# Kernel optimization log

Measured on AMD Instinct MI355X. Metric: run time of the kernel, lower is better.

## Reference

```python
import jax, jax.numpy as jnp
import numpy as np

HEADS = 8
DIM_HEAD = 64
SCALE = DIM_HEAD ** -0.5


def setup_inputs() -> dict:
    key = jax.random.key(0)
    k1, k2, k3 = jax.random.split(key, 3)
    B, N, D = 4, 2048, HEADS * DIM_HEAD  # D = inner_dim = 512
    x = jax.random.normal(k1, (B, N, D), dtype=jnp.float32)
    # nn.Linear weights stored transposed vs torch; here we use [in, out]
    w_qkv = jax.random.normal(k2, (D, 3 * D), dtype=jnp.float32) * (D ** -0.5)
    w_out = jax.random.normal(k3, (D, D), dtype=jnp.float32) * (D ** -0.5)
    b_out = jnp.zeros((D,), dtype=jnp.float32)
    return {"x": x, "w_qkv": w_qkv, "w_out": w_out, "b_out": b_out}


def reference(x, w_qkv, w_out, b_out):
    B, N, D = x.shape
    qkv = x @ w_qkv  # [B, N, 3D]
    q, k, v = jnp.split(qkv, 3, axis=-1)

    def to_heads(t):  # b n (h d) -> b h n d
        return t.reshape(B, N, HEADS, DIM_HEAD).transpose(0, 2, 1, 3)

    q, k, v = to_heads(q), to_heads(k), to_heads(v)
    dots = jnp.einsum('bhnd,bhmd->bhnm', q, k) * SCALE  # [B,H,N,N]
    attn = jax.nn.softmax(dots, axis=-1)
    out = jnp.einsum('bhnm,bhmd->bhnd', attn, v)  # [B,H,N,d]
    out = out.transpose(0, 2, 1, 3).reshape(B, N, D)  # b h n d -> b n (h d)
    return out @ w_out + b_out
```

## Files before the change

### kernel.cpp

```cpp
#include <hip/hip_runtime.h>

typedef __bf16 bf16;
typedef __bf16 bf16x8 __attribute__((ext_vector_type(8)));
typedef __bf16 bf16x4 __attribute__((ext_vector_type(4)));
typedef float f32x4 __attribute__((ext_vector_type(4)));
typedef float f32x16 __attribute__((ext_vector_type(16)));
typedef unsigned int uint2v __attribute__((ext_vector_type(2)));

#define MFMA16(a, b, c) __builtin_amdgcn_mfma_f32_16x16x32_bf16(a, b, c, 0, 0, 0)
#define MFMA32(a, b, c) __builtin_amdgcn_mfma_f32_32x32x16_bf16(a, b, c, 0, 0, 0)

#define CS 0.18033688011112042f

#if __has_builtin(__builtin_amdgcn_exp2f)
#define EXP2(x) __builtin_amdgcn_exp2f(x)
#else
#define EXP2(x) exp2f(x)
#endif

#define WAIT_VM0() __builtin_amdgcn_s_waitcnt(0x0F70)
#define WAIT_VM3() __builtin_amdgcn_s_waitcnt(0x0F73)
#define WAIT_VM4() __builtin_amdgcn_s_waitcnt(0x0F74)
#define WAIT_VM6() __builtin_amdgcn_s_waitcnt(0x0F76)
#define WAIT_VM8() __builtin_amdgcn_s_waitcnt(0x0F78)

#define BARRIER() __builtin_amdgcn_s_barrier()
#define CFENCE() asm volatile("" ::: "memory")

__device__ __forceinline__ void load_lds16(const bf16* g, bf16* l) {
    __builtin_amdgcn_global_load_lds(
        (const __attribute__((address_space(1))) unsigned int*)g,
        (__attribute__((address_space(3))) unsigned int*)l, 16, 0, 0);
}

#if __has_builtin(__builtin_amdgcn_permlane32_swap)
__device__ __forceinline__ bf16x8 build_bfrag(bf16x4 plo, bf16x4 phi, int ) {
    union { bf16x4 b; unsigned int i[2]; } ul, uh;
    ul.b = plo; uh.b = phi;
    uint2v r0 = __builtin_amdgcn_permlane32_swap(ul.i[0], uh.i[0], false, false);
    uint2v r1 = __builtin_amdgcn_permlane32_swap(ul.i[1], uh.i[1], false, false);
    union { unsigned int i[4]; bf16x8 b; } ub;
    ub.i[0] = r0[0]; ub.i[1] = r1[0]; ub.i[2] = r0[1]; ub.i[3] = r1[1];
    return ub.b;
}

__device__ __forceinline__ float sum_halves(float x) {
    union { float f; unsigned int u; } a; a.f = x;
    uint2v r = __builtin_amdgcn_permlane32_swap(a.u, a.u, false, false);
    union { unsigned int u; float f; } b0, b1;
    b0.u = r[0]; b1.u = r[1];
    return b0.f + b1.f;
}
#else
__device__ __forceinline__ bf16x4 shfl_xor32_b64(bf16x4 v) {
    union { bf16x4 b; int i[2]; } u;
    u.b = v;
    u.i[0] = __shfl_xor(u.i[0], 32, 64);
    u.i[1] = __shfl_xor(u.i[1], 32, 64);
    return u.b;
}
__device__ __forceinline__ bf16x8 build_bfrag(bf16x4 plo, bf16x4 phi, int h) {
    bf16x4 xlo = shfl_xor32_b64(plo);
    bf16x4 xhi = shfl_xor32_b64(phi);
    bf16x4 lo4 = h ? xhi : plo;
    bf16x4 hi4 = h ? phi : xlo;
    bf16x8 bb;
#pragma unroll
    for (int i = 0; i < 4; ++i) { bb[i] = lo4[i]; bb[4 + i] = hi4[i]; }
    return bb;
}
__device__ __forceinline__ float sum_halves(float x) {
    return x + __shfl_xor(x, 32, 64);
}
#endif

__global__ __launch_bounds__(256) void prep_kernel(const float* __restrict__ x,
                                                   const float* __restrict__ w_qkv,
                                                   const float* __restrict__ w_out,
                                                   bf16* __restrict__ xb,
                                                   bf16* __restrict__ wqkvT,
                                                   bf16* __restrict__ woutT) {
    __shared__ float tile[32][33];
    int bid = blockIdx.x, t = threadIdx.x;
    if (bid < 4096) {
        int i = (bid * 256 + t) * 4;
        float4 v = *(const float4*)&x[i];
        bf16x4 o = {(bf16)v.x, (bf16)v.y, (bf16)v.z, (bf16)v.w};
        *(bf16x4*)&xb[i] = o;
        return;
    }
    const float* in; bf16* out; int C, bx, by;
    if (bid < 4864) { int b2 = bid - 4096; in = w_qkv; out = wqkvT; C = 1536; bx = b2 % 48; by = b2 / 48; }
    else            { int b3 = bid - 4864; in = w_out; out = woutT; C = 512;  bx = b3 & 15; by = b3 >> 4; }
    const int R = 512;
    int tx = t & 31, ty = t >> 5;
    int c0 = bx * 32, r0 = by * 32;
#pragma unroll
    for (int i = ty; i < 32; i += 8)
        tile[i][tx] = in[(size_t)(r0 + i) * C + c0 + tx];
    __syncthreads();
#pragma unroll
    for (int i = ty; i < 32; i += 8)
        out[(size_t)(c0 + i) * R + r0 + tx] = (bf16)tile[tx][i];
}

template <int MT, int BK, int NBUF, int MODE, typename OutT>
__global__ __launch_bounds__(256, 2)
void gemm_bt_kernel(const bf16* __restrict__ A,
                    const bf16* __restrict__ Bt,
                    const float* __restrict__ bias,
                    OutT* __restrict__ C,
                    bf16* __restrict__ vtout,
                    int M, int N, int K) {
    const int BM = MT * 32;
    const int CPR = BK / 8;
    const int ASZ = BM * BK, BSZ = 128 * BK;
    const int ALD = ASZ / 2048, BLD = BSZ / 2048;
    const int L = ALD + BLD;
    __shared__ bf16 As[NBUF * ASZ];
    __shared__ bf16 Bs[NBUF * BSZ];
    int t = threadIdx.x;
    int lane = t & 63, w = t >> 6;
    int wr = w >> 1, wc = w & 1;
    int quad = lane >> 4, r16 = lane & 15;

    int lin = blockIdx.y * gridDim.x + blockIdx.x;
    int cpx = (gridDim.x * gridDim.y) >> 3;
    int nl = (lin & 7) * cpx + (lin >> 3);
    int bx = nl % gridDim.x, by = nl / gridDim.x;
    int m0 = by * BM, n0 = bx * 128;

    const f32x4 fzero = {0.f, 0.f, 0.f, 0.f};
    f32x4 acc[MT][4];
#pragma unroll
    for (int i = 0; i < MT; ++i)
#pragma unroll
        for (int j = 0; j < 4; ++j) acc[i][j] = fzero;

    const bf16* ap[ALD]; bf16* ad[ALD];
    const bf16* bp[BLD]; bf16* bd[BLD];
#pragma unroll
    for (int i = 0; i < ALD; ++i) {
        int ci = i * 256 + t;
        int row = ci / CPR, cp = ci % CPR, cc = cp ^ (row & (CPR - 1));
        ap[i] = &A[(size_t)(m0 + row) * K + cc * 8];
        ad[i] = &As[ci * 8];
    }
#pragma unroll
    for (int i = 0; i < BLD; ++i) {
        int ci = i * 256 + t;
        int row = ci / CPR, cp = ci % CPR, cc = cp ^ (row & (CPR - 1));
        bp[i] = &Bt[(size_t)(n0 + row) * K + cc * 8];
        bd[i] = &Bs[ci * 8];
    }

    auto stage = [&](int par) {
#pragma unroll
        for (int i = 0; i < ALD; ++i) { load_lds16(ap[i], ad[i] + par * ASZ); ap[i] += BK; }
#pragma unroll
        for (int i = 0; i < BLD; ++i) { load_lds16(bp[i], bd[i] + par * BSZ); bp[i] += BK; }
    };

    int nk = K / BK;
#pragma unroll
    for (int p = 0; p < NBUF - 1; ++p) stage(p);
    int cur = 0, nxt = NBUF - 1;
    for (int kk = 0; kk < nk; ++kk) {
        int rem = nk - 1 - kk;
        if (rem >= NBUF - 1) {
            stage(nxt);
            nxt = (nxt + 1 == NBUF) ? 0 : nxt + 1;
            if constexpr (L * (NBUF - 1) == 3) WAIT_VM3();
            else if constexpr (L * (NBUF - 1) == 4) WAIT_VM4();
            else if constexpr (L * (NBUF - 1) == 6) WAIT_VM6();
            else WAIT_VM8();
        } else if (NBUF == 3 && rem == 1) {
            if constexpr (L == 3) WAIT_VM3(); else WAIT_VM4();
        } else {
            WAIT_VM0();
        }
        CFENCE(); BARRIER(); CFENCE();

        const bf16* Asb = &As[cur * ASZ];
        const bf16* Bsb = &Bs[cur * BSZ];
#pragma unroll
        for (int ks = 0; ks < BK / 32; ++ks) {
            bf16x8 af[MT], bfr[4];
            int swz = (ks * 4 + quad) ^ (r16 & (CPR - 1));
#pragma unroll
            for (int mt = 0; mt < MT; ++mt)
                af[mt] = *(const bf16x8*)&Asb[(wr * (BM / 2) + mt * 16 + r16) * BK + swz * 8];
#pragma unroll
            for (int nt = 0; nt < 4; ++nt)
                bfr[nt] = *(const bf16x8*)&Bsb[(wc * 64 + nt * 16 + r16) * BK + swz * 8];
#pragma unroll
            for (int mt = 0; mt < MT; ++mt)
#pragma unroll
                for (int nt = 0; nt < 4; ++nt)
                    acc[mt][nt] = MFMA16(af[mt], bfr[nt], acc[mt][nt]);
        }
        cur = (cur + 1 == NBUF) ? 0 : cur + 1;
        if (kk + 1 < nk) { CFENCE(); BARRIER(); CFENCE(); }
    }
#pragma unroll
    for (int mt = 0; mt < MT; ++mt)
#pragma unroll
        for (int nt = 0; nt < 4; ++nt) {
            int col = n0 + wc * 64 + nt * 16 + r16;
            int row0 = m0 + wr * (BM / 2) + mt * 16 + quad * 4;
            if (MODE == 1 && n0 >= 1024) {
                int dg = col - 1024, hh = dg >> 6, d = dg & 63;
                int bb = row0 >> 11, n = row0 & 2047;
                bf16x4 o;
#pragma unroll
                for (int r = 0; r < 4; ++r) o[r] = (bf16)acc[mt][nt][r];
                *(bf16x4*)&vtout[((size_t)((bb << 3) | hh) * 64 + d) * 2048 + n] = o;
            } else {
#pragma unroll
                for (int r = 0; r < 4; ++r) {
                    float v = acc[mt][nt][r];
                    if (MODE == 1 && n0 < 512) v *= CS;
                    if (MODE == 2) v += bias[col];
                    C[(size_t)(row0 + r) * N + col] = (OutT)v;
                }
            }
        }
}

__global__ __launch_bounds__(128, 2) void attn_kernel(const bf16* __restrict__ qkv,
                                                      const bf16* __restrict__ vt,
                                                      bf16* __restrict__ out) {
    __shared__ __align__(16) char smemraw[32768];
    bf16* stage = (bf16*)smemraw;

    int t = threadIdx.x;
    int lane = t & 63, w = t >> 6;
    int h = lane >> 5, q = lane & 31;
    int bh = blockIdx.y, b = bh >> 3, hd = bh & 7;
    int qb = blockIdx.x * 64;

    bf16x8 qf[2][4];
#pragma unroll
    for (int sub = 0; sub < 2; ++sub) {
        size_t qoff = (size_t)(b * 2048 + qb + sub * 32 + q) * 1536 + hd * 64;
#pragma unroll
        for (int s = 0; s < 4; ++s)
            qf[sub][s] = *(const bf16x8*)&qkv[qoff + s * 16 + h * 8];
    }

    f32x16 o_acc[2][2];
#pragma unroll
    for (int sub = 0; sub < 2; ++sub)
#pragma unroll
        for (int db = 0; db < 2; ++db)
#pragma unroll
            for (int i = 0; i < 16; ++i) o_acc[sub][db][i] = 0.f;
    float psum[2] = {0.f, 0.f};

    bf16* base = stage + w * 8192;

    const bf16* kp[4]; const bf16* vp[4];
    int kdo[4], vdo[4];
#pragma unroll
    for (int rdd = 0; rdd < 4; ++rdd) {
        int ciK = rdd * 64 + lane;
        int rowK = ciK >> 3, ccK = (ciK & 7) ^ (rowK & 7);
        kp[rdd] = &qkv[(size_t)(b * 2048 + w * 1024 + rowK) * 1536 + 512 + hd * 64 + ccK * 8];
        kdo[rdd] = ciK * 8;
        int ciV = rdd * 64 + lane;
        int rowV = ciV >> 2, ccV = (ciV & 3) ^ (rowV & 3);
        vp[rdd] = &vt[(size_t)(bh * 64 + rowV) * 2048 + w * 1024 + ccV * 8];
        vdo[rdd] = 2048 + ciV * 8;
    }

#pragma unroll
    for (int rdd = 0; rdd < 4; ++rdd) {
        load_lds16(kp[rdd], base + kdo[rdd]);  kp[rdd] += (size_t)32 * 1536;
        load_lds16(vp[rdd], base + vdo[rdd]);  vp[rdd] += 32;
    }

    for (int it = 0; it < 32; ++it) {
        const bf16* Ks = base + (it & 1) * 4096;
        const bf16* Vs = Ks + 2048;
        if (it < 31) {
            bf16* nb = base + ((it + 1) & 1) * 4096;
#pragma unroll
            for (int rdd = 0; rdd < 4; ++rdd) {
                load_lds16(kp[rdd], nb + kdo[rdd]);  kp[rdd] += (size_t)32 * 1536;
                load_lds16(vp[rdd], nb + vdo[rdd]);  vp[rdd] += 32;
            }
            WAIT_VM8();
        } else {
            WAIT_VM0();
        }

        bf16x8 kf[4];
#pragma unroll
        for (int s = 0; s < 4; ++s) {
            int cp = (s * 2 + h) ^ (q & 7);
            kf[s] = *(const bf16x8*)&Ks[q * 64 + cp * 8];
        }
        bf16x8 vf[2][2];
#pragma unroll
        for (int kstep = 0; kstep < 2; ++kstep)
#pragma unroll
            for (int db = 0; db < 2; ++db) {
                int cp = (kstep * 2 + h) ^ (q & 3);
                vf[kstep][db] = *(const bf16x8*)&Vs[(db * 32 + q) * 32 + cp * 8];
            }

#pragma unroll
        for (int sub = 0; sub < 2; ++sub) {
            f32x16 sacc;
#pragma unroll
            for (int i = 0; i < 16; ++i) sacc[i] = 0.f;
#pragma unroll
            for (int s = 0; s < 4; ++s)
                sacc = MFMA32(kf[s], qf[sub][s], sacc);

            bf16x4 pk[4];
            float ps0 = 0.f, ps1 = 0.f, ps2 = 0.f, ps3 = 0.f;
#pragma unroll
            for (int i = 0; i < 4; ++i) {
                float p0 = EXP2(sacc[i]);
                float p1 = EXP2(sacc[4 + i]);
                float p2 = EXP2(sacc[8 + i]);
                float p3 = EXP2(sacc[12 + i]);
                ps0 += p0; ps1 += p1; ps2 += p2; ps3 += p3;
                pk[0][i] = (bf16)p0; pk[1][i] = (bf16)p1;
                pk[2][i] = (bf16)p2; pk[3][i] = (bf16)p3;
            }
            psum[sub] += (ps0 + ps1) + (ps2 + ps3);
            bf16x8 bfr0 = build_bfrag(pk[0], pk[1], h);
            bf16x8 bfr1 = build_bfrag(pk[2], pk[3], h);

#pragma unroll
            for (int db = 0; db < 2; ++db) {
                o_acc[sub][db] = MFMA32(vf[0][db], bfr0, o_acc[sub][db]);
                o_acc[sub][db] = MFMA32(vf[1][db], bfr1, o_acc[sub][db]);
            }
        }
    }

    float l_own[2];
#pragma unroll
    for (int sub = 0; sub < 2; ++sub)
        l_own[sub] = sum_halves(psum[sub]);

    __syncthreads();
    float* Of = (float*)smemraw;
    float* Lf = (float*)(smemraw + 17408);

    if (w == 1) {
#pragma unroll
        for (int sub = 0; sub < 2; ++sub) {
#pragma unroll
            for (int db = 0; db < 2; ++db)
#pragma unroll
                for (int r = 0; r < 16; ++r) {
                    int d = db * 32 + (r & 3) + 8 * (r >> 2) + 4 * h;
                    Of[(sub * 32 + q) * 68 + d] = o_acc[sub][db][r];
                }
            if (h == 0) Lf[sub * 32 + q] = l_own[sub];
        }
    }
    __syncthreads();
    if (w == 0) {
#pragma unroll
        for (int sub = 0; sub < 2; ++sub) {
#pragma unroll
            for (int db = 0; db < 2; ++db)
#pragma unroll
                for (int r = 0; r < 16; ++r) {
                    int d = db * 32 + (r & 3) + 8 * (r >> 2) + 4 * h;
                    Of[(sub * 32 + q) * 68 + d] += o_acc[sub][db][r];
                }
            if (h == 0) Lf[sub * 32 + q] += l_own[sub];
        }
    }
    __syncthreads();

    {
        int row = t >> 1, half = t & 1;
        float linv = 1.f / Lf[row];
        const float* src = &Of[row * 68 + half * 32];
        bf16* dst = &out[(size_t)(b * 2048 + qb + row) * 512 + hd * 64 + half * 32];
#pragma unroll
        for (int i = 0; i < 4; ++i) {
            f32x4 a = *(const f32x4*)&src[i * 8];
            f32x4 c = *(const f32x4*)&src[i * 8 + 4];
            bf16x8 o8;
#pragma unroll
            for (int j = 0; j < 4; ++j) {
                o8[j] = (bf16)(a[j] * linv);
                o8[4 + j] = (bf16)(c[j] * linv);
            }
            *(bf16x8*)&dst[i * 8] = o8;
        }
    }
}

extern "C" void kernel_launch(void* const* d_in, const int* in_sizes, int n_in,
                              void* d_out, int out_size, void* d_ws, size_t ws_size,
                              hipStream_t stream) {
    const float* x     = (const float*)d_in[0];
    const float* w_qkv = (const float*)d_in[1];
    const float* w_out = (const float*)d_in[2];
    const float* b_out = (const float*)d_in[3];
    float* out = (float*)d_out;

    char* ws = (char*)d_ws;
    size_t off = 0;
    bf16* xb    = (bf16*)(ws + off); off += (size_t)8192 * 512 * 2;
    bf16* wqkvT = (bf16*)(ws + off); off += (size_t)1536 * 512 * 2;
    bf16* woutT = (bf16*)(ws + off); off += (size_t)512 * 512 * 2;
    bf16* qkv   = (bf16*)(ws + off); off += (size_t)8192 * 1536 * 2;
    bf16* vt    = (bf16*)(ws + off); off += (size_t)32 * 64 * 2048 * 2;
    bf16* attn  = (bf16*)(ws + off);

    prep_kernel<<<5120, 256, 0, stream>>>(x, w_qkv, w_out, xb, wqkvT, woutT);
    gemm_bt_kernel<4, 32, 3, 1, bf16><<<dim3(12, 64), 256, 0, stream>>>(
        xb, wqkvT, nullptr, qkv, vt, 8192, 1536, 512);
    attn_kernel<<<dim3(32, 32), 128, 0, stream>>>(qkv, vt, attn);
    gemm_bt_kernel<2, 64, 2, 2, float><<<dim3(4, 128), 256, 0, stream>>>(
        attn, woutT, b_out, out, nullptr, 8192, 512, 512);
}
```

Before: 150.6 us.

## Fuse fp32-to-bf16 conversion of x into QKV GEMM A-tile loading

Removes the separate pass that converts x to bf16 in the prep kernel. A new QKV GEMM kernel reads fp32 x straight into registers, converts it, and writes swizzled bf16 A tiles to LDS, while B tiles still arrive through direct global-to-LDS loads in a two-buffer pipeline. This saves writing and re-reading the 8 MB bf16 copy of x, but each GEMM tile now reads x in fp32 (twice the bytes) and adds register staging and conversion work.

```diff
diff --git a/kernel.cpp b/kernel.cpp
--- a/kernel.cpp
+++ b/kernel.cpp
@@ -23,6 +23,7 @@
 #define WAIT_VM4() __builtin_amdgcn_s_waitcnt(0x0F74)
 #define WAIT_VM6() __builtin_amdgcn_s_waitcnt(0x0F76)
 #define WAIT_VM8() __builtin_amdgcn_s_waitcnt(0x0F78)
+#define WAIT_LGKM0() __builtin_amdgcn_s_waitcnt(0xC07F)
 
 #define BARRIER() __builtin_amdgcn_s_barrier()
 #define CFENCE() asm volatile("" ::: "memory")
@@ -31,6 +32,13 @@
     __builtin_amdgcn_global_load_lds(
         (const __attribute__((address_space(1))) unsigned int*)g,
         (__attribute__((address_space(3))) unsigned int*)l, 16, 0, 0);
+}
+
+__device__ __forceinline__ bf16x8 cvt8(float4 a, float4 b) {
+    bf16x8 o;
+    o[0] = (bf16)a.x; o[1] = (bf16)a.y; o[2] = (bf16)a.z; o[3] = (bf16)a.w;
+    o[4] = (bf16)b.x; o[5] = (bf16)b.y; o[6] = (bf16)b.z; o[7] = (bf16)b.w;
+    return o;
 }
 
 #if __has_builtin(__builtin_amdgcn_permlane32_swap)
@@ -74,24 +82,15 @@
 }
 #endif
 
-__global__ __launch_bounds__(256) void prep_kernel(const float* __restrict__ x,
-                                                   const float* __restrict__ w_qkv,
+__global__ __launch_bounds__(256) void prep_kernel(const float* __restrict__ w_qkv,
                                                    const float* __restrict__ w_out,
-                                                   bf16* __restrict__ xb,
                                                    bf16* __restrict__ wqkvT,
                                                    bf16* __restrict__ woutT) {
     __shared__ float tile[32][33];
     int bid = blockIdx.x, t = threadIdx.x;
-    if (bid < 4096) {
-        int i = (bid * 256 + t) * 4;
-        float4 v = *(const float4*)&x[i];
-        bf16x4 o = {(bf16)v.x, (bf16)v.y, (bf16)v.z, (bf16)v.w};
-        *(bf16x4*)&xb[i] = o;
-        return;
-    }
     const float* in; bf16* out; int C, bx, by;
-    if (bid < 4864) { int b2 = bid - 4096; in = w_qkv; out = wqkvT; C = 1536; bx = b2 % 48; by = b2 / 48; }
-    else            { int b3 = bid - 4864; in = w_out; out = woutT; C = 512;  bx = b3 & 15; by = b3 >> 4; }
+    if (bid < 768) { in = w_qkv; out = wqkvT; C = 1536; bx = bid % 48; by = bid / 48; }
+    else           { int b3 = bid - 768; in = w_out; out = woutT; C = 512; bx = b3 & 15; by = b3 >> 4; }
     const int R = 512;
     int tx = t & 31, ty = t >> 5;
     int c0 = bx * 32, r0 = by * 32;
@@ -102,6 +101,133 @@
 #pragma unroll
     for (int i = ty; i < 32; i += 8)
         out[(size_t)(c0 + i) * R + r0 + tx] = (bf16)tile[tx][i];
+}
+
+__global__ __launch_bounds__(256, 2) void gemm_qkv_kernel(const float* __restrict__ X,
+                                                          const bf16* __restrict__ Bt,
+                                                          bf16* __restrict__ C,
+                                                          bf16* __restrict__ vtout) {
+    const int Kd = 512, Nd = 1536;
+    const int ASZ = 128 * 32, BSZ = 128 * 32;
+    __shared__ bf16 As[2 * ASZ];
+    __shared__ bf16 Bs[2 * BSZ];
+    int t = threadIdx.x;
+    int lane = t & 63, w = t >> 6;
+    int wr = w >> 1, wc = w & 1;
+    int quad = lane >> 4, r16 = lane & 15;
+
+    int lin = blockIdx.y * gridDim.x + blockIdx.x;
+    int cpx = (gridDim.x * gridDim.y) >> 3;
+    int nl = (lin & 7) * cpx + (lin >> 3);
+    int bx = nl % gridDim.x, by = nl / gridDim.x;
+    int m0 = by * 128, n0 = bx * 128;
+
+    const f32x4 fzero = {0.f, 0.f, 0.f, 0.f};
+    f32x4 acc[4][4];
+#pragma unroll
+    for (int i = 0; i < 4; ++i)
+#pragma unroll
+        for (int j = 0; j < 4; ++j) acc[i][j] = fzero;
+
+    const float* apf[2]; bf16* adw[2];
+#pragma unroll
+    for (int i = 0; i < 2; ++i) {
+        int ci = i * 256 + t;
+        int row = ci >> 2, cp = ci & 3, cc = cp ^ (row & 3);
+        apf[i] = &X[(size_t)(m0 + row) * Kd + cc * 8];
+        adw[i] = &As[ci * 8];
+    }
+    const bf16* bp[2]; bf16* bd[2];
+#pragma unroll
+    for (int i = 0; i < 2; ++i) {
+        int ci = i * 256 + t;
+        int row = ci >> 2, cp = ci & 3, cc = cp ^ (row & 3);
+        bp[i] = &Bt[(size_t)(n0 + row) * Kd + cc * 8];
+        bd[i] = &Bs[ci * 8];
+    }
+
+#define LOADA(r0, r1, r2, r3)                                          \
+    {                                                                  \
+        r0 = *(const float4*)apf[0]; r1 = *(const float4*)(apf[0] + 4);\
+        r2 = *(const float4*)apf[1]; r3 = *(const float4*)(apf[1] + 4);\
+        apf[0] += 32; apf[1] += 32;                                    \
+    }
+#define ISSUEB(par)                                                    \
+    {                                                                  \
+        load_lds16(bp[0], bd[0] + (par)*BSZ); bp[0] += 32;             \
+        load_lds16(bp[1], bd[1] + (par)*BSZ); bp[1] += 32;             \
+    }
+#define COMPUTE(par)                                                   \
+    {                                                                  \
+        bf16x8 af[4], bfr[4];                                          \
+        int swz = quad ^ (r16 & 3);                                    \
+        _Pragma("unroll")                                              \
+        for (int mt = 0; mt < 4; ++mt)                                 \
+            af[mt] = *(const bf16x8*)&As[(par)*ASZ + (wr * 64 + mt * 16 + r16) * 32 + swz * 8]; \
+        _Pragma("unroll")                                              \
+        for (int nt = 0; nt < 4; ++nt)                                 \
+            bfr[nt] = *(const bf16x8*)&Bs[(par)*BSZ + (wc * 64 + nt * 16 + r16) * 32 + swz * 8]; \
+        _Pragma("unroll")                                              \
+        for (int mt = 0; mt < 4; ++mt)                                 \
+            _Pragma("unroll")                                          \
+            for (int nt = 0; nt < 4; ++nt)                             \
+                acc[mt][nt] = MFMA16(af[mt], bfr[nt], acc[mt][nt]);    \
+    }
+
+    float4 a0, a1, a2, a3;
+    float4 b0, b1, b2, b3;
+
+    LOADA(a0, a1, a2, a3);
+    ISSUEB(0);
+#pragma unroll 1
+    for (int kk = 0; kk < 16; kk += 2) {
+        LOADA(b0, b1, b2, b3);
+        ISSUEB(1);
+        WAIT_VM6();
+        *(bf16x8*)(adw[0]) = cvt8(a0, a1);
+        *(bf16x8*)(adw[1]) = cvt8(a2, a3);
+        CFENCE(); WAIT_LGKM0(); CFENCE(); BARRIER(); CFENCE();
+        COMPUTE(0);
+        CFENCE(); BARRIER(); CFENCE();
+        if (kk + 2 < 16) {
+            LOADA(a0, a1, a2, a3);
+            ISSUEB(0);
+            WAIT_VM6();
+        } else {
+            WAIT_VM0();
+        }
+        *(bf16x8*)(adw[0] + ASZ) = cvt8(b0, b1);
+        *(bf16x8*)(adw[1] + ASZ) = cvt8(b2, b3);
+        CFENCE(); WAIT_LGKM0(); CFENCE(); BARRIER(); CFENCE();
+        COMPUTE(1);
+        if (kk + 2 < 16) { CFENCE(); BARRIER(); CFENCE(); }
+    }
+#undef LOADA
+#undef ISSUEB
+#undef COMPUTE
+
+#pragma unroll
+    for (int mt = 0; mt < 4; ++mt)
+#pragma unroll
+        for (int nt = 0; nt < 4; ++nt) {
+            int col = n0 + wc * 64 + nt * 16 + r16;
+            int row0 = m0 + wr * 64 + mt * 16 + quad * 4;
+            if (n0 >= 1024) {
+                int dg = col - 1024, hh = dg >> 6, d = dg & 63;
+                int bb = row0 >> 11, n = row0 & 2047;
+                bf16x4 o;
+#pragma unroll
+                for (int r = 0; r < 4; ++r) o[r] = (bf16)acc[mt][nt][r];
+                *(bf16x4*)&vtout[((size_t)((bb << 3) | hh) * 64 + d) * 2048 + n] = o;
+            } else {
+#pragma unroll
+                for (int r = 0; r < 4; ++r) {
+                    float v = acc[mt][nt][r];
+                    if (n0 < 512) v *= CS;
+                    C[(size_t)(row0 + r) * Nd + col] = (bf16)v;
+                }
+            }
+        }
 }
 
 template <int MT, int BK, int NBUF, int MODE, typename OutT>
@@ -411,16 +537,14 @@
 
     char* ws = (char*)d_ws;
     size_t off = 0;
-    bf16* xb    = (bf16*)(ws + off); off += (size_t)8192 * 512 * 2;
     bf16* wqkvT = (bf16*)(ws + off); off += (size_t)1536 * 512 * 2;
     bf16* woutT = (bf16*)(ws + off); off += (size_t)512 * 512 * 2;
     bf16* qkv   = (bf16*)(ws + off); off += (size_t)8192 * 1536 * 2;
     bf16* vt    = (bf16*)(ws + off); off += (size_t)32 * 64 * 2048 * 2;
     bf16* attn  = (bf16*)(ws + off);
 
-    prep_kernel<<<5120, 256, 0, stream>>>(x, w_qkv, w_out, xb, wqkvT, woutT);
-    gemm_bt_kernel<4, 32, 3, 1, bf16><<<dim3(12, 64), 256, 0, stream>>>(
-        xb, wqkvT, nullptr, qkv, vt, 8192, 1536, 512);
+    prep_kernel<<<1024, 256, 0, stream>>>(w_qkv, w_out, wqkvT, woutT);
+    gemm_qkv_kernel<<<dim3(12, 64), 256, 0, stream>>>(x, wqkvT, qkv, vt);
     attn_kernel<<<dim3(32, 32), 128, 0, stream>>>(qkv, vt, attn);
     gemm_bt_kernel<2, 64, 2, 2, float><<<dim3(4, 128), 256, 0, stream>>>(
         attn, woutT, b_out, out, nullptr, 8192, 512, 512);
```

New measurement: 151.5 us. About the same (+0.6%).
